# Optimization experiments

Measured on AMD Instinct MI355X. Metric: run time of the kernel, lower is better.

The kernel has to match this reference:

```python
import jax, jax.numpy as jnp
import numpy as np

P_FACTOR = 3.0
EPS = 1e-12  # torch F.normalize eps


def _l2_normalize(x):
    # matches torch.nn.functional.normalize(x, dim=-1): x / max(||x||, eps)
    n = jnp.linalg.norm(x, axis=-1, keepdims=True)
    return x / jnp.maximum(n, EPS)


def setup_inputs() -> dict:
    key = jax.random.key(0)
    k1, k2, k3 = jax.random.split(key, 3)
    N, D, H, C = 8192, 16384, 256, 28
    return {
        "features": jax.random.normal(k1, (N, H), dtype=jnp.float32),
        "ex_features": jax.random.normal(k2, (D, H), dtype=jnp.float32),
        "ex_class_reps": jax.random.normal(k3, (D, C), dtype=jnp.float32),
    }


def reference(features, ex_features, ex_class_reps):
    # cosine similarity: [N, D]
    s = _l2_normalize(features) @ _l2_normalize(ex_features).T
    # power-law activation: |s|^p * sign(s)
    a = jnp.power(jnp.abs(s), P_FACTOR) * jnp.sign(s)
    intensity = a.sum(axis=1)               # [N]
    echo = a @ ex_class_reps                # [N, C]
    return (echo, intensity)
```

## Files before the change

### kernel.cpp

```cpp
#include <hip/hip_runtime.h>
#include <stdint.h>


typedef unsigned short u16;
typedef __bf16 bf16x8 __attribute__((ext_vector_type(8)));
typedef float f32x4 __attribute__((ext_vector_type(4)));
typedef unsigned short u16x4 __attribute__((ext_vector_type(4)));

#define NQ 8192
#define ND 16384
#define NH 256
#define NC 28
#define DCHUNK 2048
#define NDT 32
#define NSLOT 8

__device__ __forceinline__ u16 f2bf(float f) {
  unsigned u = __builtin_bit_cast(unsigned, f);
  u += 0x7fffu + ((u >> 16) & 1u);
  return (u16)(u >> 16);
}

__device__ __forceinline__ unsigned cvtpk(float lo, float hi) {
  unsigned r;
  asm("v_cvt_pk_bf16_f32 %0, %1, %2" : "=v"(r) : "v"(lo), "v"(hi));
  return r;
}

__device__ __forceinline__ void swap2(unsigned& x, unsigned& y) {
  asm("v_permlane32_swap_b32 %0, %1" : "+v"(x), "+v"(y));
  asm("v_permlane16_swap_b32 %0, %1" : "+v"(x), "+v"(y));
}

__device__ __forceinline__ void gload16(const void* g, void* l) {
  __builtin_amdgcn_global_load_lds(
      (__attribute__((address_space(1))) void*)g,
      (__attribute__((address_space(3))) void*)l, 16, 0, 0);
}

__global__ __launch_bounds__(256) void prep_kernel(
    const float* __restrict__ feat, const float* __restrict__ exf,
    const float* __restrict__ V, u16* __restrict__ qn, u16* __restrict__ kn,
    u16* __restrict__ Vt) {
  if (blockIdx.x < 6144) {
    const int wid = threadIdx.x >> 6, lane = threadIdx.x & 63;
    const int row = blockIdx.x * 4 + wid;
    const float* in = (row < NQ) ? feat + (size_t)row * NH
                                 : exf + (size_t)(row - NQ) * NH;
    u16* out = (row < NQ) ? qn + (size_t)row * NH : kn + (size_t)(row - NQ) * NH;
    float4 v = ((const float4*)in)[lane];
    float ss = v.x * v.x + v.y * v.y + v.z * v.z + v.w * v.w;
#pragma unroll
    for (int m = 1; m <= 32; m <<= 1) ss += __shfl_xor(ss, m, 64);
    const float sc = 1.0f / fmaxf(sqrtf(ss), 1e-12f);
    u16x4 o;
    o.x = f2bf(v.x * sc); o.y = f2bf(v.y * sc);
    o.z = f2bf(v.z * sc); o.w = f2bf(v.w * sc);
    *(u16x4*)(out + lane * 4) = o;
  } else {
    const int d = (blockIdx.x - 6144) * 256 + threadIdx.x;
#pragma unroll
    for (int c = 0; c < NC; ++c) Vt[(size_t)c * ND + d] = f2bf(V[(size_t)d * NC + c]);
    Vt[(size_t)28 * ND + d] = 0x3F80;
    Vt[(size_t)29 * ND + d] = 0;
    Vt[(size_t)30 * ND + d] = 0;
    Vt[(size_t)31 * ND + d] = 0;
  }
}

__global__ __launch_bounds__(512, 4) void fused_kernel(
    const u16* __restrict__ Qn, const u16* __restrict__ Kn,
    const u16* __restrict__ Vt, float* __restrict__ ep) {
  __shared__ alignas(16) char smem[32768];
  const int tid = threadIdx.x;
  const int wid = tid >> 6;
  const int lane = tid & 63;
  const int l16 = lane & 15;
  const int lg = lane >> 4;
  const int wr = wid >> 1;
  const int wd = wid & 1;
  const int dch = blockIdx.x & 7;
  const int ntile = blockIdx.x >> 3;
  const int rowbase = ntile * 128 + wr * 32;

  bf16x8 qA[2][8];
#pragma unroll
  for (int mb = 0; mb < 2; ++mb)
#pragma unroll
    for (int ks = 0; ks < 8; ++ks)
      qA[mb][ks] = *(const bf16x8*)(Qn + (size_t)(rowbase + mb * 16 + l16) * NH +
                                    ks * 32 + lg * 8);

  f32x4 eacc[2][2];
#pragma unroll
  for (int mb = 0; mb < 2; ++mb) {
    eacc[mb][0] = f32x4{0.f, 0.f, 0.f, 0.f};
    eacc[mb][1] = f32x4{0.f, 0.f, 0.f, 0.f};
  }
  f32x4 sacc[2][2];

  const u16* kc = Kn + (size_t)dch * DCHUNK * NH;
  const int srow = (wid & 3) * 16 + (lane >> 2);
  const u16* kb = kc + (size_t)srow * NH + ((lane & 3) ^ ((lane >> 3) & 3)) * 8;
  const int ssbase = (wid >> 2) * 32;

  auto stage = [&](int buf, const u16* src0) {
#pragma unroll
    for (int j = 0; j < 2; ++j)
      gload16(src0 + ssbase + j * 64,
              smem + buf * 16384 + j * 8192 + wid * 1024);
  };

  const int rsw = (l16 >> 1) & 3;

  auto compute = [&](int buf, int h) {
    const char* kbuf = smem + buf * 16384;
#pragma unroll
    for (int k2 = 0; k2 < 4; ++k2) {
      bf16x8 B[2];
#pragma unroll
      for (int nb = 0; nb < 2; ++nb)
        B[nb] = *(const bf16x8*)(kbuf + k2 * 4096 + (wd * 32 + nb * 16 + l16) * 64 +
                                 ((lg ^ rsw) << 4));
      __builtin_amdgcn_s_setprio(1);
#pragma unroll
      for (int mb = 0; mb < 2; ++mb)
#pragma unroll
        for (int nb = 0; nb < 2; ++nb)
          sacc[mb][nb] = __builtin_amdgcn_mfma_f32_16x16x32_bf16(
              B[nb], qA[mb][h * 4 + k2], sacc[mb][nb], 0, 0, 0);
      __builtin_amdgcn_s_setprio(0);
    }
  };

  stage(0, kb);
  __syncthreads();

  for (int t = 0; t < NDT; ++t) {
    const size_t toff = (size_t)t * 64 * NH;
    const int dbase = dch * DCHUNK + t * 64 + wd * 32;

#pragma unroll
    for (int mb = 0; mb < 2; ++mb) {
      sacc[mb][0] = f32x4{0.f, 0.f, 0.f, 0.f};
      sacc[mb][1] = f32x4{0.f, 0.f, 0.f, 0.f};
    }

    stage(1, kb + toff + 128);
    compute(0, 0);
    __syncthreads();

    bf16x8 vB[2];
#pragma unroll
    for (int cn = 0; cn < 2; ++cn)
      vB[cn] = *(const bf16x8*)(Vt + (size_t)(cn * 16 + l16) * ND + dbase + lg * 8);

    if (t < NDT - 1) stage(0, kb + toff + 64 * NH);
    compute(1, 1);

#pragma unroll
    for (int mb = 0; mb < 2; ++mb) {
      f32x4 sx = sacc[mb][0];
      f32x4 sy = sacc[mb][1];
      f32x4 cx = sx * sx * sx;
      f32x4 cy = sy * sy * sy;
      unsigned x0 = cvtpk(cx[0], cx[1]);
      unsigned x1 = cvtpk(cx[2], cx[3]);
      unsigned y0 = cvtpk(cy[0], cy[1]);
      unsigned y1 = cvtpk(cy[2], cy[3]);
      swap2(x0, y0);
      swap2(x1, y1);
      const int4 ai = {(int)x0, (int)x1, (int)y0, (int)y1};
      const bf16x8 aA = __builtin_bit_cast(bf16x8, ai);
#pragma unroll
      for (int cn = 0; cn < 2; ++cn)
        eacc[mb][cn] = __builtin_amdgcn_mfma_f32_16x16x32_bf16(
            aA, vB[cn], eacc[mb][cn], 0, 0, 0);
    }

    __syncthreads();
  }

  float* eml = (float*)smem;
  if (wd == 1) {
    float* dst = eml + (wr * 64 + lane) * 18;
#pragma unroll
    for (int mb = 0; mb < 2; ++mb)
#pragma unroll
      for (int cn = 0; cn < 2; ++cn)
        *(f32x4*)(dst + (mb * 2 + cn) * 4) = eacc[mb][cn];
  }
  __syncthreads();
  if (wd == 0) {
    const float* src = eml + (wr * 64 + lane) * 18;
#pragma unroll
    for (int mb = 0; mb < 2; ++mb)
#pragma unroll
      for (int cn = 0; cn < 2; ++cn) {
        const f32x4 m = eacc[mb][cn] + *(const f32x4*)(src + (mb * 2 + cn) * 4);
#pragma unroll
        for (int r = 0; r < 4; ++r) {
          const int row = rowbase + mb * 16 + lg * 4 + r;
          ep[((size_t)dch * NQ + row) * 32 + cn * 16 + l16] = m[r];
        }
      }
  }
}

__global__ __launch_bounds__(256) void reduce_kernel(const float* __restrict__ ep,
                                                     float* __restrict__ out) {
  const int g = blockIdx.x * 256 + threadIdx.x;
  const int q = g >> 5, c = g & 31;
  if (c < NC) {
    float s = 0.f;
#pragma unroll
    for (int k = 0; k < NSLOT; ++k) s += ep[((size_t)k * NQ + q) * 32 + c];
    out[(size_t)q * NC + c] = s;
  } else if (c == NC) {
    float s = 0.f;
#pragma unroll
    for (int k = 0; k < NSLOT; ++k) s += ep[((size_t)k * NQ + q) * 32 + NC];
    out[(size_t)NQ * NC + q] = s;
  }
}

extern "C" void kernel_launch(void* const* d_in, const int* in_sizes, int n_in,
                              void* d_out, int out_size, void* d_ws, size_t ws_size,
                              hipStream_t stream) {
  const float* feat = (const float*)d_in[0];
  const float* exf  = (const float*)d_in[1];
  const float* exc  = (const float*)d_in[2];
  float* out = (float*)d_out;
  char* ws = (char*)d_ws;
  u16* qn = (u16*)ws;
  u16* kn = (u16*)(ws + 4194304);
  u16* vt = (u16*)(ws + 12582912);
  float* ep = (float*)(ws + 13631488);

  prep_kernel<<<dim3(6208), dim3(256), 0, stream>>>(feat, exf, exc, qn, kn, vt);
  fused_kernel<<<dim3(512), dim3(512), 0, stream>>>(qn, kn, vt, ep);
  reduce_kernel<<<dim3(NQ * 32 / 256), dim3(256), 0, stream>>>(ep, out);
}
```

Baseline: 88.53 us.

## Split each block's D-tile across four waves per row group with 1024 threads

```diff
diff --git a/kernel.cpp b/kernel.cpp
--- a/kernel.cpp
+++ b/kernel.cpp
@@ -13,7 +13,7 @@
 #define NC 28
 #define DCHUNK 2048
 #define NDT 32
-#define NSLOT 8
+#define NSLOT 16
 
 __device__ __forceinline__ u16 f2bf(float f) {
   unsigned u = __builtin_bit_cast(unsigned, f);
@@ -68,7 +68,7 @@
   }
 }
 
-__global__ __launch_bounds__(512, 4) void fused_kernel(
+__global__ __launch_bounds__(1024, 4) void fused_kernel(
     const u16* __restrict__ Qn, const u16* __restrict__ Kn,
     const u16* __restrict__ Vt, float* __restrict__ ep) {
   __shared__ alignas(16) char smem[32768];
@@ -77,8 +77,8 @@
   const int lane = tid & 63;
   const int l16 = lane & 15;
   const int lg = lane >> 4;
-  const int wr = wid >> 1;
-  const int wd = wid & 1;
+  const int wr = wid >> 2;
+  const int wd = wid & 3;
   const int dch = blockIdx.x & 7;
   const int ntile = blockIdx.x >> 3;
   const int rowbase = ntile * 128 + wr * 32;
@@ -97,18 +97,15 @@
     eacc[mb][0] = f32x4{0.f, 0.f, 0.f, 0.f};
     eacc[mb][1] = f32x4{0.f, 0.f, 0.f, 0.f};
   }
-  f32x4 sacc[2][2];
+  f32x4 sacc[2];
 
   const u16* kc = Kn + (size_t)dch * DCHUNK * NH;
-  const int srow = (wid & 3) * 16 + (lane >> 2);
-  const u16* kb = kc + (size_t)srow * NH + ((lane & 3) ^ ((lane >> 3) & 3)) * 8;
-  const int ssbase = (wid >> 2) * 32;
+  const int srow = (tid >> 2) & 63;
+  const u16* kb = kc + (size_t)srow * NH + ((tid & 3) ^ ((tid >> 3) & 3)) * 8 +
+                  (tid >> 8) * 32;
 
   auto stage = [&](int buf, const u16* src0) {
-#pragma unroll
-    for (int j = 0; j < 2; ++j)
-      gload16(src0 + ssbase + j * 64,
-              smem + buf * 16384 + j * 8192 + wid * 1024);
+    gload16(src0, smem + buf * 16384 + wid * 1024);
   };
 
   const int rsw = (l16 >> 1) & 3;
@@ -117,18 +114,13 @@
     const char* kbuf = smem + buf * 16384;
 #pragma unroll
     for (int k2 = 0; k2 < 4; ++k2) {
-      bf16x8 B[2];
-#pragma unroll
-      for (int nb = 0; nb < 2; ++nb)
-        B[nb] = *(const bf16x8*)(kbuf + k2 * 4096 + (wd * 32 + nb * 16 + l16) * 64 +
-                                 ((lg ^ rsw) << 4));
+      const bf16x8 B = *(const bf16x8*)(kbuf + k2 * 4096 + (wd * 16 + l16) * 64 +
+                                        ((lg ^ rsw) << 4));
       __builtin_amdgcn_s_setprio(1);
 #pragma unroll
       for (int mb = 0; mb < 2; ++mb)
-#pragma unroll
-        for (int nb = 0; nb < 2; ++nb)
-          sacc[mb][nb] = __builtin_amdgcn_mfma_f32_16x16x32_bf16(
-              B[nb], qA[mb][h * 4 + k2], sacc[mb][nb], 0, 0, 0);
+        sacc[mb] = __builtin_amdgcn_mfma_f32_16x16x32_bf16(
+            B, qA[mb][h * 4 + k2], sacc[mb], 0, 0, 0);
       __builtin_amdgcn_s_setprio(0);
     }
   };
@@ -138,36 +130,31 @@
 
   for (int t = 0; t < NDT; ++t) {
     const size_t toff = (size_t)t * 64 * NH;
-    const int dbase = dch * DCHUNK + t * 64 + wd * 32;
-
-#pragma unroll
-    for (int mb = 0; mb < 2; ++mb) {
-      sacc[mb][0] = f32x4{0.f, 0.f, 0.f, 0.f};
-      sacc[mb][1] = f32x4{0.f, 0.f, 0.f, 0.f};
-    }
+    const int dbase = dch * DCHUNK + t * 64 + wd * 16;
+
+    sacc[0] = f32x4{0.f, 0.f, 0.f, 0.f};
+    sacc[1] = f32x4{0.f, 0.f, 0.f, 0.f};
 
     stage(1, kb + toff + 128);
     compute(0, 0);
     __syncthreads();
 
-    bf16x8 vB[2];
-#pragma unroll
-    for (int cn = 0; cn < 2; ++cn)
-      vB[cn] = *(const bf16x8*)(Vt + (size_t)(cn * 16 + l16) * ND + dbase + lg * 8);
-
     if (t < NDT - 1) stage(0, kb + toff + 64 * NH);
     compute(1, 1);
 
+    bf16x8 vB[2];
+#pragma unroll
+    for (int cn = 0; cn < 2; ++cn)
+      vB[cn] = *(const bf16x8*)(Vt + (size_t)(cn * 16 + l16) * ND + dbase +
+                                (lg & 1) * 8);
+
 #pragma unroll
     for (int mb = 0; mb < 2; ++mb) {
-      f32x4 sx = sacc[mb][0];
-      f32x4 sy = sacc[mb][1];
+      f32x4 sx = sacc[mb];
       f32x4 cx = sx * sx * sx;
-      f32x4 cy = sy * sy * sy;
       unsigned x0 = cvtpk(cx[0], cx[1]);
       unsigned x1 = cvtpk(cx[2], cx[3]);
-      unsigned y0 = cvtpk(cy[0], cy[1]);
-      unsigned y1 = cvtpk(cy[2], cy[3]);
+      unsigned y0 = 0, y1 = 0;
       swap2(x0, y0);
       swap2(x1, y1);
       const int4 ai = {(int)x0, (int)x1, (int)y0, (int)y1};
@@ -182,8 +169,8 @@
   }
 
   float* eml = (float*)smem;
-  if (wd == 1) {
-    float* dst = eml + (wr * 64 + lane) * 18;
+  if (wd & 1) {
+    float* dst = eml + (((wd >> 1) * 4 + wr) * 64 + lane) * 16;
 #pragma unroll
     for (int mb = 0; mb < 2; ++mb)
 #pragma unroll
@@ -191,8 +178,9 @@
         *(f32x4*)(dst + (mb * 2 + cn) * 4) = eacc[mb][cn];
   }
   __syncthreads();
-  if (wd == 0) {
-    const float* src = eml + (wr * 64 + lane) * 18;
+  if (!(wd & 1)) {
+    const float* src = eml + (((wd >> 1) * 4 + wr) * 64 + lane) * 16;
+    const int slot = dch * 2 + (wd >> 1);
 #pragma unroll
     for (int mb = 0; mb < 2; ++mb)
 #pragma unroll
@@ -201,7 +189,7 @@
 #pragma unroll
         for (int r = 0; r < 4; ++r) {
           const int row = rowbase + mb * 16 + lg * 4 + r;
-          ep[((size_t)dch * NQ + row) * 32 + cn * 16 + l16] = m[r];
+          ep[((size_t)slot * NQ + row) * 32 + cn * 16 + l16] = m[r];
         }
       }
   }
@@ -238,6 +226,6 @@
   float* ep = (float*)(ws + 13631488);
 
   prep_kernel<<<dim3(6208), dim3(256), 0, stream>>>(feat, exf, exc, qn, kn, vt);
-  fused_kernel<<<dim3(512), dim3(512), 0, stream>>>(qn, kn, vt, ep);
+  fused_kernel<<<dim3(512), dim3(1024), 0, stream>>>(qn, kn, vt, ep);
   reduce_kernel<<<dim3(NQ * 32 / 256), dim3(256), 0, stream>>>(ep, out);
 }
```

Result: slower. 155.1 us (+75.2%).
